# Kernel tuning notes

Hardware: AMD Instinct MI355X
Metric: run time of the kernel (lower is better)

## Reference

```python
import jax, jax.numpy as jnp
import numpy as np

NUM_LEVELS = 4
RADIUS = 4


def _avg_pool2(x):
    # x: [N, H, W] -> 2x2 avg pool, stride 2, VALID (matches F.avg_pool2d(corr, 2, 2))
    s = jax.lax.reduce_window(x, 0.0, jax.lax.add, (1, 2, 2), (1, 2, 2), 'VALID')
    return s * 0.25


def _bilinear_sampler(img, coords):
    # img: [N, H, W]; coords: [N, K, K, 2] with (x, y) in pixel units.
    # Matches grid_sample(align_corners=True, padding_mode='zeros').
    N, H, W = img.shape
    x, y = coords[..., 0], coords[..., 1]
    x0 = jnp.floor(x)
    y0 = jnp.floor(y)
    nidx = jnp.arange(N)[:, None, None]

    def corner(xi, yi, w):
        valid = (xi >= 0) & (xi <= W - 1) & (yi >= 0) & (yi <= H - 1)
        xc = jnp.clip(xi, 0, W - 1).astype(jnp.int32)
        yc = jnp.clip(yi, 0, H - 1).astype(jnp.int32)
        return jnp.where(valid, img[nidx, yc, xc], 0.0) * w

    wx1 = x - x0
    wx0 = 1.0 - wx1
    wy1 = y - y0
    wy0 = 1.0 - wy1
    return (corner(x0, y0, wx0 * wy0) + corner(x0 + 1.0, y0, wx1 * wy0)
            + corner(x0, y0 + 1.0, wx0 * wy1) + corner(x0 + 1.0, y0 + 1.0, wx1 * wy1))


def setup_inputs() -> dict:
    key = jax.random.key(0)
    ks = jax.random.split(key, 8)
    B, C, H, W, D = 2, 256, 46, 96, 256
    fmap1 = jax.random.normal(ks[0], (B, C, H, W), jnp.float32)
    fmap2 = jax.random.normal(ks[1], (B, C, H, W), jnp.float32)
    ys, xs = jnp.meshgrid(jnp.arange(H, dtype=jnp.float32),
                          jnp.arange(W, dtype=jnp.float32), indexing='ij')
    base = jnp.broadcast_to(jnp.stack([xs, ys], 0), (B, 2, H, W))  # channels = (x, y)
    coords1 = base
    coords_lookup = base + 2.0 * jax.random.normal(ks[2], (B, 2, H, W), jnp.float32)
    Wf = jax.random.normal(ks[3], (C, D), jnp.float32) / np.sqrt(C).astype(np.float32)
    bf = jnp.zeros((D,), jnp.float32)
    Wpos = jax.random.normal(ks[4], (2, D), jnp.float32) * 0.003
    Wq = jax.random.normal(ks[5], (D, D), jnp.float32) / np.sqrt(D).astype(np.float32)
    Wk = jax.random.normal(ks[6], (D, D), jnp.float32) / np.sqrt(D).astype(np.float32)
    return {"fmap1": fmap1, "fmap2": fmap2, "coords1": coords1,
            "coords_lookup": coords_lookup, "Wf": Wf, "bf": bf,
            "Wpos": Wpos, "Wq": Wq, "Wk": Wk}


def reference(fmap1, fmap2, coords1, coords_lookup, Wf, bf, Wpos, Wq, Wk):
    B, C, H, W = fmap1.shape
    HW = H * W
    D = Wf.shape[1]
    dt = fmap1.dtype
    # --- update(): SETrans cross-attention correlation volume ---
    # coords2 = gen_all_indices -> full (y, x) grid
    ys, xs = jnp.meshgrid(jnp.arange(H, dtype=dt), jnp.arange(W, dtype=dt), indexing='ij')
    coords2_yx = jnp.broadcast_to(jnp.stack([ys, xs], -1), (B, H, W, 2)).reshape(B, HW, 2)
    # coords1 stored as (x, y) channels; permute(0,2,3,1).flip(-1) -> (y, x)
    coords1_yx = jnp.transpose(coords1, (0, 2, 3, 1))[..., ::-1].reshape(B, HW, 2)
    f1 = jnp.transpose(fmap1.reshape(B, C, HW), (0, 2, 1))  # [B, HW, C]
    f2 = jnp.transpose(fmap2.reshape(B, C, HW), (0, 2, 1))
    pos1 = coords1_yx @ Wpos                                  # [B, HW, D]
    pos2 = coords2_yx @ Wpos
    vispos1 = f1 @ Wf + bf + pos1
    vispos2 = f2 @ Wf + bf + pos2
    scale = jnp.sqrt(jnp.asarray(D, dt))
    pos_biases = jnp.einsum('bid,bjd->bij', pos1, pos2) / scale  # injected positional biases
    q = vispos1 @ Wq
    k = vispos2 @ Wk
    scores = jnp.einsum('bid,bjd->bij', q, k) / scale + pos_biases
    corr = jax.nn.softmax(scores, axis=-1)                    # [B, HW1, HW2] attn-prob correlation
    corr = corr.reshape(B * HW, H, W)
    pyramid = [corr]
    for _ in range(NUM_LEVELS - 1):
        corr = _avg_pool2(corr)
        pyramid.append(corr)
    # --- __call__(coords): multiscale bilinear lookup ---
    r = RADIUS
    d = jnp.linspace(-r, r, 2 * r + 1, dtype=dt)
    dyy, dxx = jnp.meshgrid(d, d, indexing='ij')              # matches torch.meshgrid(dy, dx)
    delta = jnp.stack([dyy, dxx], -1)[None]                   # [1, K, K, 2]
    cl = jnp.transpose(coords_lookup, (0, 2, 3, 1)).reshape(B * HW, 1, 1, 2)
    outs = []
    for i, lvl in enumerate(pyramid):
        coords_lvl = cl / (2.0 ** i) + delta                  # [B*HW, K, K, 2]
        samp = _bilinear_sampler(lvl, coords_lvl)             # [B*HW, K, K]
        outs.append(samp.reshape(B, H, W, -1))
    out = jnp.concatenate(outs, axis=-1)                      # [B, H, W, L*K*K]
    return jnp.transpose(out, (0, 3, 1, 2)).astype(jnp.float32)
```

## Files before the change

kernel.cpp:

```cpp
#include <hip/hip_runtime.h>
#include <cstdint>

typedef _Float16 f16;
typedef __attribute__((ext_vector_type(2))) _Float16 f16x2;
typedef __attribute__((ext_vector_type(4))) _Float16 f16x4;
typedef __attribute__((ext_vector_type(8))) _Float16 f16x8;
typedef __attribute__((ext_vector_type(4))) float f32x4;

#define NB 2
#define NH 46
#define NW 96
#define NHW 4416
#define ND 256
#define NTILES 276
#define SSTR 4424
#define L2E 1.44269504f

#define OFF_WFQ 0
#define OFF_WFK 131072
#define OFF_PQ  262144
#define OFF_PK  264192
#define OFF_BQ  266240
#define OFF_BK  267264
#define OFF_GS  268288
#define OFF_Q   268544
#define OFF_K   4790528
#define OFF_RM  9312512
#define OFF_S   9453824
#define SCOL    4432
#define WS_NEED 87740672UL

__global__ __launch_bounds__(256) void prep_kernel(
    const float* __restrict__ Wf, const float* __restrict__ bf,
    const float* __restrict__ Wpos, const float* __restrict__ Wq,
    const float* __restrict__ Wk, char* __restrict__ ws) {
  f16* WFQ = (f16*)(ws + OFF_WFQ);
  f16* WFK = (f16*)(ws + OFF_WFK);
  float* PQ = (float*)(ws + OFF_PQ);
  float* PK = (float*)(ws + OFF_PK);
  float* BQ = (float*)(ws + OFF_BQ);
  float* BK = (float*)(ws + OFF_BK);
  float* GS = (float*)(ws + OFF_GS);
  int bid = blockIdx.x, d = threadIdx.x;
  if (bid < 256) {
    int c = bid;
    float aq = 0.f, ak = 0.f;
#pragma unroll 8
    for (int t = 0; t < 256; ++t) {
      float wf = Wf[c * 256 + t];
      aq += wf * Wq[t * 256 + d];
      ak += wf * Wk[t * 256 + d];
    }
    WFQ[c * 256 + d] = (f16)(aq * 0.0625f);
    WFK[c * 256 + d] = (f16)ak;
  } else if (bid == 256) {
    float pq0 = 0, pq1 = 0, pk0 = 0, pk1 = 0, bq = 0, bk = 0;
#pragma unroll 4
    for (int c = 0; c < 256; ++c) {
      float wq = Wq[c * 256 + d], wk = Wk[c * 256 + d];
      pq0 += Wpos[c] * wq;       pq1 += Wpos[256 + c] * wq;
      pk0 += Wpos[c] * wk;       pk1 += Wpos[256 + c] * wk;
      bq  += bf[c] * wq;         bk  += bf[c] * wk;
    }
    PQ[d] = pq0 * 0.0625f; PQ[256 + d] = pq1 * 0.0625f;
    PK[d] = pk0;           PK[256 + d] = pk1;
    BQ[d] = bq * 0.0625f;  BK[d] = bk;
  } else if (d < 4) {
    int a = d >> 1, b2 = d & 1;
    float g = 0;
    for (int t = 0; t < 256; ++t) g += Wpos[a * 256 + t] * Wpos[b2 * 256 + t];
    GS[d] = g * 0.0625f;
  }
}

__global__ __launch_bounds__(256, 2) void qk_gemm(
    const float* __restrict__ fmap1, const float* __restrict__ fmap2,
    const float* __restrict__ coords1, char* __restrict__ ws) {
  __shared__ f16 As[64 * 40];
  __shared__ f16 Bs[256 * 40];
  __shared__ float py[64], px[64];
  const int z = blockIdx.z;
  const float* fmap = z ? fmap2 : fmap1;
  const f16* Wt = (const f16*)(ws + (z ? OFF_WFK : OFF_WFQ));
  const float* P = (const float*)(ws + (z ? OFF_PK : OFF_PQ));
  const float* bias = (const float*)(ws + (z ? OFF_BK : OFF_BQ));
  f16* outb = (f16*)(ws + (z ? OFF_K : OFF_Q));
  const int t = threadIdx.x;
  const int g0 = blockIdx.x * 64;
  const int b = g0 / NHW;
  const int hwb = g0 - b * NHW;
  if (t < 64) {
    int hw = hwb + t;
    if (z == 0) {
      py[t] = coords1[(b * 2 + 1) * NHW + hw];
      px[t] = coords1[(b * 2 + 0) * NHW + hw];
    } else {
      int y = hw / NW;
      py[t] = (float)y;
      px[t] = (float)(hw - y * NW);
    }
  }
  const int lane = t & 63, wave = t >> 6;
  const int wr = (wave >> 1) * 32, wc0 = (wave & 1) * 128;
  const int hwl = t & 63, cl0 = t >> 6;
  const int dd = t & 127, ch = t >> 7;
  f32x4 acc[2][8] = {};
  for (int kt = 0; kt < 8; ++kt) {
    int kk = kt * 32;
    __syncthreads();
#pragma unroll
    for (int i = 0; i < 8; ++i) {
      int c = cl0 + i * 4;
      As[hwl * 40 + c] = (f16)fmap[(size_t)(b * ND + kk + c) * NHW + hwb + hwl];
    }
#pragma unroll
    for (int i = 0; i < 16; ++i) {
      int c = ch * 16 + i;
      Bs[dd * 40 + c] = Wt[(kk + c) * ND + dd];
      Bs[(dd + 128) * 40 + c] = Wt[(kk + c) * ND + dd + 128];
    }
    __syncthreads();
    int row = lane & 15, kq = (lane >> 4) * 8;
    f16x8 a0 = *(const f16x8*)&As[(wr + row) * 40 + kq];
    f16x8 a1 = *(const f16x8*)&As[(wr + 16 + row) * 40 + kq];
#pragma unroll
    for (int s = 0; s < 8; ++s) {
      f16x8 bs = *(const f16x8*)&Bs[(wc0 + 16 * s + row) * 40 + kq];
      acc[0][s] = __builtin_amdgcn_mfma_f32_16x16x32_f16(a0, bs, acc[0][s], 0, 0, 0);
      acc[1][s] = __builtin_amdgcn_mfma_f32_16x16x32_f16(a1, bs, acc[1][s], 0, 0, 0);
    }
  }
#pragma unroll
  for (int fi = 0; fi < 2; ++fi)
#pragma unroll
    for (int s = 0; s < 8; ++s)
#pragma unroll
      for (int r = 0; r < 4; ++r) {
        int rowl = wr + fi * 16 + (lane >> 4) * 4 + r;
        int d = wc0 + s * 16 + (lane & 15);
        float v = acc[fi][s][r] + bias[d] + py[rowl] * P[d] + px[rowl] * P[ND + d];
        outb[(size_t)(g0 + rowl) * ND + d] = (f16)v;
      }
}

__global__ __launch_bounds__(384, 1) void score_gemm(
    const float* __restrict__ coords1, char* __restrict__ ws) {
  __shared__ f16 kls[2][32][264];
  __shared__ f16 stw[6][32][36];
  __shared__ float u0s[192], u1s[192];
  const int tid = threadIdx.x;
  const int blk = blockIdx.x;
  const int xcd = blk & 7;
  const int b = xcd >> 2, nq = xcd & 3;
  const int hw0 = (blk >> 3) * 192;
  const int j00 = nq * 1104;
  const float* GS = (const float*)(ws + OFF_GS);
  if (tid < 192) {
    int hw = hw0 + tid;
    float cy = coords1[(b * 2 + 1) * NHW + hw];
    float cx = coords1[(b * 2 + 0) * NHW + hw];
    u0s[tid] = cy * GS[0] + cx * GS[2];
    u1s[tid] = cy * GS[1] + cx * GS[3];
  }
  const f16* __restrict__ qb = (const f16*)(ws + OFF_Q);
  const f16* __restrict__ kb = (const f16*)(ws + OFF_K);
  f16* __restrict__ gSb = (f16*)(ws + OFF_S) + ((size_t)b * NHW + hw0) * SCOL;
  float* __restrict__ rmG = (float*)(ws + OFF_RM);
  const int lane = tid & 63, wave = tid >> 6;
  const int q = lane & 15, h = lane >> 4;
  const int wq0 = wave * 32;
  f16x8 qfrag[2][8];
#pragma unroll
  for (int s = 0; s < 2; ++s)
#pragma unroll
    for (int ks = 0; ks < 8; ++ks)
      qfrag[s][ks] = *(const f16x8*)&qb[(size_t)(b * NHW + hw0 + wq0 + s * 16 + q) * ND + ks * 32 + h * 8];
  for (int c = tid; c < 32 * 32; c += 384) {
    int r = c >> 5, cc = c & 31;
    *(f16x8*)&kls[0][r][cc * 8] =
        *(const f16x8*)&kb[(size_t)(b * NHW + j00 + r) * ND + cc * 8];
  }
  __syncthreads();
  const float u0a = u0s[wq0 + q], u1a = u1s[wq0 + q];
  const float u0b = u0s[wq0 + 16 + q], u1b = u1s[wq0 + 16 + q];
  float pmax0 = -3e38f, pmax1 = -3e38f;
  const int srow = lane >> 1, scg = lane & 1;

  for (int it = 0; it <= 34; ++it) {
    const int buf = it & 1;
    const int jp = j00 + it * 32;
    const bool full = (it < 34);
    if (it < 34) {
      const int nW = (it < 33) ? 32 : 16;
      const int jn = j00 + (it + 1) * 32;
      for (int c = tid; c < nW * 32; c += 384) {
        int r = c >> 5, cc = c & 31;
        *(f16x8*)&kls[buf ^ 1][r][cc * 8] =
            *(const f16x8*)&kb[(size_t)(b * NHW + jn + r) * ND + cc * 8];
      }
    }
    f32x4 acc00 = {}, acc01 = {}, acc10 = {}, acc11 = {};
#pragma unroll
    for (int ks = 0; ks < 8; ++ks) {
      f16x8 kf = *(const f16x8*)&kls[buf][q][ks * 32 + h * 8];
      acc00 = __builtin_amdgcn_mfma_f32_16x16x32_f16(kf, qfrag[0][ks], acc00, 0, 0, 0);
      acc01 = __builtin_amdgcn_mfma_f32_16x16x32_f16(kf, qfrag[1][ks], acc01, 0, 0, 0);
    }
    if (full) {
#pragma unroll
      for (int ks = 0; ks < 8; ++ks) {
        f16x8 kf = *(const f16x8*)&kls[buf][16 + q][ks * 32 + h * 8];
        acc10 = __builtin_amdgcn_mfma_f32_16x16x32_f16(kf, qfrag[0][ks], acc10, 0, 0, 0);
        acc11 = __builtin_amdgcn_mfma_f32_16x16x32_f16(kf, qfrag[1][ks], acc11, 0, 0, 0);
      }
    }
    {
      float yf0[4], xf0[4];
#pragma unroll
      for (int r = 0; r < 4; ++r) {
        int j = jp + h * 4 + r;
        int yj = j / NW;
        yf0[r] = (float)yj; xf0[r] = (float)(j - yj * NW);
      }
      f16x4 va, vb;
#pragma unroll
      for (int r = 0; r < 4; ++r) {
        float s0 = acc00[r] + u0a * yf0[r] + u1a * xf0[r];
        float s1 = acc01[r] + u0b * yf0[r] + u1b * xf0[r];
        pmax0 = fmaxf(pmax0, s0);
        pmax1 = fmaxf(pmax1, s1);
        va[r] = (f16)s0; vb[r] = (f16)s1;
      }
      *(f16x4*)&stw[wave][q][h * 4] = va;
      *(f16x4*)&stw[wave][16 + q][h * 4] = vb;
      if (full) {
        float yf1[4], xf1[4];
#pragma unroll
        for (int r = 0; r < 4; ++r) {
          int j = jp + 16 + h * 4 + r;
          int yj = j / NW;
          yf1[r] = (float)yj; xf1[r] = (float)(j - yj * NW);
        }
#pragma unroll
        for (int r = 0; r < 4; ++r) {
          float s0 = acc10[r] + u0a * yf1[r] + u1a * xf1[r];
          float s1 = acc11[r] + u0b * yf1[r] + u1b * xf1[r];
          pmax0 = fmaxf(pmax0, s0);
          pmax1 = fmaxf(pmax1, s1);
          va[r] = (f16)s0; vb[r] = (f16)s1;
        }
        *(f16x4*)&stw[wave][q][16 + h * 4] = va;
        *(f16x4*)&stw[wave][16 + q][16 + h * 4] = vb;
      }
    }
    if (full) {
      f16x8 rA = *(const f16x8*)&stw[wave][srow][scg * 16];
      f16x8 rB = *(const f16x8*)&stw[wave][srow][scg * 16 + 8];
      f16* dst = &gSb[(size_t)(wq0 + srow) * SCOL + jp + scg * 16];
      *(f16x8*)&dst[0] = rA;
      *(f16x8*)&dst[8] = rB;
    } else {
      f16x8 rA = *(const f16x8*)&stw[wave][srow][scg * 8];
      *(f16x8*)&gSb[(size_t)(wq0 + srow) * SCOL + jp + scg * 8] = rA;
    }
    __syncthreads();
  }
  pmax0 = fmaxf(pmax0, __shfl_xor(pmax0, 16));
  pmax0 = fmaxf(pmax0, __shfl_xor(pmax0, 32));
  pmax1 = fmaxf(pmax1, __shfl_xor(pmax1, 16));
  pmax1 = fmaxf(pmax1, __shfl_xor(pmax1, 32));
  if (lane < 16) {
    rmG[((size_t)b * 4 + nq) * NHW + hw0 + wq0 + q] = pmax0;
    rmG[((size_t)b * 4 + nq) * NHW + hw0 + wq0 + 16 + q] = pmax1;
  }
}

__global__ __launch_bounds__(512) void lookup_kernel(
    const float* __restrict__ clup, const char* __restrict__ ws,
    float* __restrict__ out) {
  __shared__ f16 lv1W[8][1104];
  __shared__ f16 lv2W[8][264];
  __shared__ f16 lv3W[8][60];
  __shared__ f16 winW[8][10][24];
  const int tid = threadIdx.x;
  const int blk0 = blockIdx.x;
  const int xcd = blk0 & 7;
  const int b = xcd >> 2;
  const int hw0 = ((blk0 >> 3) * 4 + (xcd & 3)) * 16;
  const f16* gS = (const f16*)(ws + OFF_S);
  const float* rmG = (const float*)(ws + OFF_RM);
  const int lane = tid & 63, wave = tid >> 6;
  f16* lv1 = lv1W[wave];
  f16* lv2 = lv2W[wave];
  f16* lv3 = lv3W[wave];

  for (int rr2 = 0; rr2 < 2; ++rr2) {
    const int r = wave * 2 + rr2;
    const int hw = hw0 + r;
    const size_t grow = (size_t)b * NHW + hw;
    const f16* sp = gS + grow * SCOL;
    const float clx = clup[(b * 2 + 0) * NHW + hw];
    const float cly = clup[(b * 2 + 1) * NHW + hw];
    const float* rp = rmG + (size_t)b * 4 * NHW + hw;
    const float m = fmaxf(fmaxf(rp[0], rp[NHW]), fmaxf(rp[2 * NHW], rp[3 * NHW]));
    const int wy0 = (int)floorf(cly) - 4;
    const int wx0 = (int)floorf(clx) - 4;
    const int xb = (wx0 >> 3) << 3;
    if (lane < 30) {
      int r10 = lane / 3, chk = lane - r10 * 3;
      int yy = wy0 + r10;
      int xc = xb + chk * 8;
      if (yy >= 0 && yy < NH) {
        if (xc >= 0 && xc + 8 <= NW) {
          *(f16x8*)&winW[wave][r10][chk * 8] = *(const f16x8*)&sp[yy * NW + xc];
        } else {
#pragma unroll
          for (int e = 0; e < 8; ++e) {
            int x = xc + e;
            winW[wave][r10][chk * 8 + e] =
                (x >= 0 && x < NW) ? sp[yy * NW + x] : (f16)0.f;
          }
        }
      }
    }
    float psum = 0.f;
    for (int u = lane; u < 276; u += 64) {
      int y1 = u / 12, g = u - y1 * 12;
      f16x8 A = *(const f16x8*)&sp[(2 * y1) * NW + g * 8];
      f16x8 B = *(const f16x8*)&sp[(2 * y1 + 1) * NW + g * 8];
      f16x4 v;
#pragma unroll
      for (int e = 0; e < 4; ++e) {
        float e00 = __builtin_amdgcn_exp2f(((float)A[2 * e] - m) * L2E);
        float e01 = __builtin_amdgcn_exp2f(((float)A[2 * e + 1] - m) * L2E);
        float e10 = __builtin_amdgcn_exp2f(((float)B[2 * e] - m) * L2E);
        float e11 = __builtin_amdgcn_exp2f(((float)B[2 * e + 1] - m) * L2E);
        float s4 = (e00 + e01) + (e10 + e11);
        v[e] = (f16)s4;
        psum += s4;
      }
      *(f16x4*)&lv1[y1 * 48 + g * 4] = v;
    }
#pragma unroll
    for (int off = 1; off < 64; off <<= 1) psum += __shfl_xor(psum, off);
    const float rinv = 1.f / psum;
    __threadfence_block();
    for (int c2 = lane; c2 < 264; c2 += 64) {
      int yy = c2 / 24, xx = c2 - yy * 24;
      f16x2 a = *(const f16x2*)&lv1[(2 * yy) * 48 + 2 * xx];
      f16x2 bb = *(const f16x2*)&lv1[(2 * yy + 1) * 48 + 2 * xx];
      lv2[c2] = (f16)(((float)a[0] + (float)a[1]) + ((float)bb[0] + (float)bb[1]));
    }
    __threadfence_block();
    if (lane < 60) {
      int yy = lane / 12, xx = lane - yy * 12;
      f16x2 a = *(const f16x2*)&lv2[(2 * yy) * 24 + 2 * xx];
      f16x2 bb = *(const f16x2*)&lv2[(2 * yy + 1) * 24 + 2 * xx];
      lv3[lane] = (f16)(((float)a[0] + (float)a[1]) + ((float)bb[0] + (float)bb[1]));
    }
    __threadfence_block();
    for (int c = lane; c < 324; c += 64) {
      int lvl = c / 81, rem = c - lvl * 81;
      int k0 = rem / 9, k1 = rem - k0 * 9;
      const float wdiv[4] = {1.f, 0.25f, 0.0625f, 0.015625f};
      const int Wi[4] = {96, 48, 24, 12}, Hi[4] = {46, 23, 11, 5};
      float xq = clx / (float)(1 << lvl) + (float)(k0 - 4);
      float yq = cly / (float)(1 << lvl) + (float)(k1 - 4);
      float x0f = floorf(xq), y0f = floorf(yq);
      int x0 = (int)x0f, y0 = (int)y0f;
      float wx1 = xq - x0f, wx0f_ = 1.f - wx1;
      float wy1 = yq - y0f, wy0f_ = 1.f - wy1;
      int Wl = Wi[lvl], Hl = Hi[lvl];
      float v = 0.f;
#pragma unroll
      for (int dy = 0; dy < 2; ++dy)
#pragma unroll
        for (int dx = 0; dx < 2; ++dx) {
          int xi = x0 + dx, yi = y0 + dy;
          if (xi >= 0 && xi < Wl && yi >= 0 && yi < Hl) {
            float pv;
            if (lvl == 0)
              pv = __builtin_amdgcn_exp2f(
                  ((float)winW[wave][yi - wy0][xi - xb] - m) * L2E);
            else if (lvl == 1) pv = (float)lv1[yi * 48 + xi];
            else if (lvl == 2) pv = (float)lv2[yi * 24 + xi];
            else               pv = (float)lv3[yi * 12 + xi];
            v += pv * (dx ? wx1 : wx0f_) * (dy ? wy1 : wy0f_);
          }
        }
      int hh = hw / NW, wcol = hw - hh * NW;
      int chn = lvl * 81 + k0 * 9 + k1;
      out[((size_t)(b * 324 + chn) * NH + hh) * NW + wcol] = v * wdiv[lvl] * rinv;
    }
    __threadfence_block();
  }
}

__global__ __launch_bounds__(1024) void attn_lookup(
    const float* __restrict__ coords1, const float* __restrict__ clup,
    const char* __restrict__ ws, float* __restrict__ out) {
  __shared__ f16 S[16 * SSTR];
  __shared__ f16 lv1[4][1104];
  __shared__ f16 lv2[4][264];
  __shared__ f16 lv3[4][60];
  __shared__ float wmax[16][16];
  __shared__ float wpart[16];
  __shared__ float u0s[16], u1s[16], clxs[16], clys[16], rinv[16], rowmaxS[16];
  const int tid = threadIdx.x;
  const int blk0 = blockIdx.x;
  const int xcd = blk0 & 7;
  const int b = xcd >> 2;
  const int hw0 = ((blk0 >> 3) * 4 + (xcd & 3)) * 16;
  const float* GS = (const float*)(ws + OFF_GS);
  if (tid < 16) {
    int hw = hw0 + tid;
    float cy = coords1[(b * 2 + 1) * NHW + hw];
    float cx = coords1[(b * 2 + 0) * NHW + hw];
    u0s[tid] = cy * GS[0] + cx * GS[2];
    u1s[tid] = cy * GS[1] + cx * GS[3];
    clxs[tid] = clup[(b * 2 + 0) * NHW + hw];
    clys[tid] = clup[(b * 2 + 1) * NHW + hw];
  }
  const f16* qb = (const f16*)(ws + OFF_Q);
  const f16* kb = (const f16*)(ws + OFF_K);
  const int lane = tid & 63;
  const int arow = lane & 15, akq = (lane >> 4) * 8;
  const int i0 = (lane >> 4) * 4;
  f16x8 afrag[8];
#pragma unroll
  for (int ks = 0; ks < 8; ++ks)
    afrag[ks] = *(const f16x8*)&qb[(size_t)(b * NHW + hw0 + arow) * ND + ks * 32 + akq];
  __syncthreads();
  float u0r[4], u1r[4];
#pragma unroll
  for (int r = 0; r < 4; ++r) { u0r[r] = u0s[i0 + r]; u1r[r] = u1s[i0 + r]; }
  const int wave = tid >> 6;
  float pmax[4] = {-3e38f, -3e38f, -3e38f, -3e38f};
  {
    const int cnt = (NTILES - wave + 15) / 16;
    const f16* kp = &kb[(size_t)(b * NHW + wave * 16 + arow) * ND + akq];
    const size_t tstep = (size_t)256 * ND;
    int nt = wave;
    f16x8 h0[4], h1[4];
#pragma unroll
    for (int s = 0; s < 4; ++s) h0[s] = *(const f16x8*)&kp[s * 32];
    for (int i = 0; i < cnt; ++i) {
      f32x4 acc0 = {}, acc1 = {};
#pragma unroll
      for (int s = 0; s < 4; ++s) h1[s] = *(const f16x8*)&kp[128 + s * 32];
      acc0 = __builtin_amdgcn_mfma_f32_16x16x32_f16(afrag[0], h0[0], acc0, 0, 0, 0);
      acc1 = __builtin_amdgcn_mfma_f32_16x16x32_f16(afrag[1], h0[1], acc1, 0, 0, 0);
      acc0 = __builtin_amdgcn_mfma_f32_16x16x32_f16(afrag[2], h0[2], acc0, 0, 0, 0);
      acc1 = __builtin_amdgcn_mfma_f32_16x16x32_f16(afrag[3], h0[3], acc1, 0, 0, 0);
      const f16* kpn = kp + tstep;
      if (i + 1 < cnt) {
#pragma unroll
        for (int s = 0; s < 4; ++s) h0[s] = *(const f16x8*)&kpn[s * 32];
      }
      acc0 = __builtin_amdgcn_mfma_f32_16x16x32_f16(afrag[4], h1[0], acc0, 0, 0, 0);
      acc1 = __builtin_amdgcn_mfma_f32_16x16x32_f16(afrag[5], h1[1], acc1, 0, 0, 0);
      acc0 = __builtin_amdgcn_mfma_f32_16x16x32_f16(afrag[6], h1[2], acc0, 0, 0, 0);
      acc1 = __builtin_amdgcn_mfma_f32_16x16x32_f16(afrag[7], h1[3], acc1, 0, 0, 0);
      int j = nt * 16 + (lane & 15);
      int yj = j / NW;
      float yf = (float)yj, xf = (float)(j - yj * NW);
#pragma unroll
      for (int r = 0; r < 4; ++r) {
        float s = acc0[r] + acc1[r] + u0r[r] * yf + u1r[r] * xf;
        pmax[r] = fmaxf(pmax[r], s);
        S[(i0 + r) * SSTR + j] = (f16)s;
      }
      kp = kpn; nt += 16;
    }
  }
#pragma unroll
  for (int off = 1; off < 16; off <<= 1)
#pragma unroll
    for (int r = 0; r < 4; ++r) pmax[r] = fmaxf(pmax[r], __shfl_xor(pmax[r], off));
  if ((lane & 15) == 0) {
#pragma unroll
    for (int r = 0; r < 4; ++r) wmax[wave][i0 + r] = pmax[r];
  }
  __syncthreads();
  if (tid < 16) {
    float m = wmax[0][tid];
#pragma unroll
    for (int w = 1; w < 16; ++w) m = fmaxf(m, wmax[w][tid]);
    rowmaxS[tid] = m;
  }
  __syncthreads();
  const int rgrp = tid >> 8, ts = tid & 255;
  for (int p = 0; p < 4; ++p) {
    const int r = p * 4 + rgrp;
    const f16* Sr = &S[r * SSTR];
    const float m = rowmaxS[r];
    float psum = 0.f;
    for (int c = ts; c < 1104; c += 256) {
      int yy = c / 48, xx = c - yy * 48;
      f16x2 a = *(const f16x2*)&Sr[(2 * yy) * NW + 2 * xx];
      f16x2 bb = *(const f16x2*)&Sr[(2 * yy + 1) * NW + 2 * xx];
      float e0 = __builtin_amdgcn_exp2f(((float)a[0] - m) * L2E);
      float e1 = __builtin_amdgcn_exp2f(((float)a[1] - m) * L2E);
      float e2 = __builtin_amdgcn_exp2f(((float)bb[0] - m) * L2E);
      float e3 = __builtin_amdgcn_exp2f(((float)bb[1] - m) * L2E);
      float s4 = (e0 + e1) + (e2 + e3);
      lv1[rgrp][c] = (f16)s4;
      psum += s4;
    }
#pragma unroll
    for (int off = 1; off < 64; off <<= 1) psum += __shfl_xor(psum, off);
    if (lane == 0) wpart[tid >> 6] = psum;
    __syncthreads();
    if (tid < 4)
      rinv[p * 4 + tid] = 1.f / (((wpart[tid * 4] + wpart[tid * 4 + 1]) +
                                  (wpart[tid * 4 + 2] + wpart[tid * 4 + 3])));
    for (int c2 = ts; c2 < 264; c2 += 256) {
      int yy = c2 / 24, xx = c2 - yy * 24;
      f16x2 a = *(const f16x2*)&lv1[rgrp][(2 * yy) * 48 + 2 * xx];
      f16x2 bb = *(const f16x2*)&lv1[rgrp][(2 * yy + 1) * 48 + 2 * xx];
      lv2[rgrp][c2] = (f16)(((float)a[0] + (float)a[1]) + ((float)bb[0] + (float)bb[1]));
    }
    __syncthreads();
    if (ts < 60) {
      int yy = ts / 12, xx = ts - yy * 12;
      f16x2 a = *(const f16x2*)&lv2[rgrp][(2 * yy) * 24 + 2 * xx];
      f16x2 bb = *(const f16x2*)&lv2[rgrp][(2 * yy + 1) * 24 + 2 * xx];
      lv3[rgrp][ts] = (f16)(((float)a[0] + (float)a[1]) + ((float)bb[0] + (float)bb[1]));
    }
    __syncthreads();
    for (int idx = tid; idx < 1296; idx += 1024) {
      int rl = idx / 324, c = idx - rl * 324;
      int rr = p * 4 + rl;
      int lvl = c / 81, rem = c - lvl * 81;
      int k0 = rem / 9, k1 = rem - k0 * 9;
      const float wdiv[4] = {1.f, 0.25f, 0.0625f, 0.015625f};
      const int Wi[4] = {96, 48, 24, 12}, Hi[4] = {46, 23, 11, 5};
      float m2 = rowmaxS[rr];
      float xq = clxs[rr] / (float)(1 << lvl) + (float)(k0 - 4);
      float yq = clys[rr] / (float)(1 << lvl) + (float)(k1 - 4);
      float x0f = floorf(xq), y0f = floorf(yq);
      int x0 = (int)x0f, y0 = (int)y0f;
      float wx1 = xq - x0f, wx0 = 1.f - wx1;
      float wy1 = yq - y0f, wy0 = 1.f - wy1;
      int Wl = Wi[lvl], Hl = Hi[lvl];
      float v = 0.f;
#pragma unroll
      for (int dy = 0; dy < 2; ++dy)
#pragma unroll
        for (int dx = 0; dx < 2; ++dx) {
          int xi = x0 + dx, yi = y0 + dy;
          if (xi >= 0 && xi < Wl && yi >= 0 && yi < Hl) {
            float pv;
            if (lvl == 0)
              pv = __builtin_amdgcn_exp2f(((float)S[rr * SSTR + yi * NW + xi] - m2) * L2E);
            else if (lvl == 1) pv = (float)lv1[rl][yi * 48 + xi];
            else if (lvl == 2) pv = (float)lv2[rl][yi * 24 + xi];
            else               pv = (float)lv3[rl][yi * 12 + xi];
            v += pv * (dx ? wx1 : wx0) * (dy ? wy1 : wy0);
          }
        }
      int hw = hw0 + rr;
      int h = hw / NW, w = hw - h * NW;
      int chn = lvl * 81 + k0 * 9 + k1;
      out[((size_t)(b * 324 + chn) * NH + h) * NW + w] = v * wdiv[lvl] * rinv[rr];
    }
    __syncthreads();
  }
}

extern "C" void kernel_launch(void* const* d_in, const int* in_sizes, int n_in,
                              void* d_out, int out_size, void* d_ws, size_t ws_size,
                              hipStream_t stream) {
  const float* fmap1 = (const float*)d_in[0];
  const float* fmap2 = (const float*)d_in[1];
  const float* coords1 = (const float*)d_in[2];
  const float* clup = (const float*)d_in[3];
  const float* Wf = (const float*)d_in[4];
  const float* bf = (const float*)d_in[5];
  const float* Wpos = (const float*)d_in[6];
  const float* Wq = (const float*)d_in[7];
  const float* Wk = (const float*)d_in[8];
  char* ws = (char*)d_ws;
  float* out = (float*)d_out;

  prep_kernel<<<dim3(258), dim3(256), 0, stream>>>(Wf, bf, Wpos, Wq, Wk, ws);
  qk_gemm<<<dim3(138, 1, 2), dim3(256), 0, stream>>>(fmap1, fmap2, coords1, ws);
  if (ws_size >= (size_t)WS_NEED) {
    score_gemm<<<dim3(23 * 8), dim3(384), 0, stream>>>(coords1, ws);
    lookup_kernel<<<dim3(NB * NTILES), dim3(512), 0, stream>>>(clup, ws, out);
  } else {
    attn_lookup<<<dim3(NB * NTILES), dim3(1024), 0, stream>>>(coords1, clup, ws, out);
  }
}
```

Baseline: 145.6 us.

## Split score GEMM key range into eight segments and store row maxima inline

The score GEMM grid doubles from 184 to 368 blocks by splitting each batch's key columns into eight uneven tile ranges instead of four. Launch bounds now allow two blocks per CU, which should fill more of the device. The per-segment row maxima are written into padding columns of the score row rather than a separate buffer, so the lookup kernel reads them next to the scores it already loads. In exchange, each block repeats the Q-fragment loads and prologue, and the code assumes SCOL has spare space past column 4416.

```diff
diff --git a/kernel.cpp b/kernel.cpp
--- a/kernel.cpp
+++ b/kernel.cpp
@@ -143,17 +143,20 @@
       }
 }
 
-__global__ __launch_bounds__(384, 1) void score_gemm(
+__global__ __launch_bounds__(384, 2) void score_gemm(
     const float* __restrict__ coords1, char* __restrict__ ws) {
   __shared__ f16 kls[2][32][264];
   __shared__ f16 stw[6][32][36];
   __shared__ float u0s[192], u1s[192];
   const int tid = threadIdx.x;
   const int blk = blockIdx.x;
-  const int xcd = blk & 7;
-  const int b = xcd >> 2, nq = xcd & 3;
-  const int hw0 = (blk >> 3) * 192;
-  const int j00 = nq * 1104;
+  const int comb = blk & 15;
+  const int b = comb >> 3, ns = comb & 7;
+  const int hw0 = (blk >> 4) * 192;
+  const int sstart[9] = {0, 17, 34, 51, 68, 85, 102, 120, 138};
+  const int t0s = sstart[ns];
+  const int cnt = sstart[ns + 1] - t0s;
+  const int j00 = t0s * 32;
   const float* GS = (const float*)(ws + OFF_GS);
   if (tid < 192) {
     int hw = hw0 + tid;
@@ -165,7 +168,6 @@
   const f16* __restrict__ qb = (const f16*)(ws + OFF_Q);
   const f16* __restrict__ kb = (const f16*)(ws + OFF_K);
   f16* __restrict__ gSb = (f16*)(ws + OFF_S) + ((size_t)b * NHW + hw0) * SCOL;
-  float* __restrict__ rmG = (float*)(ws + OFF_RM);
   const int lane = tid & 63, wave = tid >> 6;
   const int q = lane & 15, h = lane >> 4;
   const int wq0 = wave * 32;
@@ -186,14 +188,12 @@
   float pmax0 = -3e38f, pmax1 = -3e38f;
   const int srow = lane >> 1, scg = lane & 1;
 
-  for (int it = 0; it <= 34; ++it) {
+  for (int it = 0; it < cnt; ++it) {
     const int buf = it & 1;
     const int jp = j00 + it * 32;
-    const bool full = (it < 34);
-    if (it < 34) {
-      const int nW = (it < 33) ? 32 : 16;
+    if (it + 1 < cnt) {
       const int jn = j00 + (it + 1) * 32;
-      for (int c = tid; c < nW * 32; c += 384) {
+      for (int c = tid; c < 1024; c += 384) {
         int r = c >> 5, cc = c & 31;
         *(f16x8*)&kls[buf ^ 1][r][cc * 8] =
             *(const f16x8*)&kb[(size_t)(b * NHW + jn + r) * ND + cc * 8];
@@ -206,21 +206,22 @@
       acc00 = __builtin_amdgcn_mfma_f32_16x16x32_f16(kf, qfrag[0][ks], acc00, 0, 0, 0);
       acc01 = __builtin_amdgcn_mfma_f32_16x16x32_f16(kf, qfrag[1][ks], acc01, 0, 0, 0);
     }
-    if (full) {
-#pragma unroll
-      for (int ks = 0; ks < 8; ++ks) {
-        f16x8 kf = *(const f16x8*)&kls[buf][16 + q][ks * 32 + h * 8];
-        acc10 = __builtin_amdgcn_mfma_f32_16x16x32_f16(kf, qfrag[0][ks], acc10, 0, 0, 0);
-        acc11 = __builtin_amdgcn_mfma_f32_16x16x32_f16(kf, qfrag[1][ks], acc11, 0, 0, 0);
-      }
+#pragma unroll
+    for (int ks = 0; ks < 8; ++ks) {
+      f16x8 kf = *(const f16x8*)&kls[buf][16 + q][ks * 32 + h * 8];
+      acc10 = __builtin_amdgcn_mfma_f32_16x16x32_f16(kf, qfrag[0][ks], acc10, 0, 0, 0);
+      acc11 = __builtin_amdgcn_mfma_f32_16x16x32_f16(kf, qfrag[1][ks], acc11, 0, 0, 0);
     }
     {
-      float yf0[4], xf0[4];
+      float yf0[4], xf0[4], yf1[4], xf1[4];
 #pragma unroll
       for (int r = 0; r < 4; ++r) {
         int j = jp + h * 4 + r;
         int yj = j / NW;
         yf0[r] = (float)yj; xf0[r] = (float)(j - yj * NW);
+        int j1 = jp + 16 + h * 4 + r;
+        int yj1 = j1 / NW;
+        yf1[r] = (float)yj1; xf1[r] = (float)(j1 - yj1 * NW);
       }
       f16x4 va, vb;
 #pragma unroll
@@ -233,35 +234,23 @@
       }
       *(f16x4*)&stw[wave][q][h * 4] = va;
       *(f16x4*)&stw[wave][16 + q][h * 4] = vb;
-      if (full) {
-        float yf1[4], xf1[4];
-#pragma unroll
-        for (int r = 0; r < 4; ++r) {
-          int j = jp + 16 + h * 4 + r;
-          int yj = j / NW;
-          yf1[r] = (float)yj; xf1[r] = (float)(j - yj * NW);
-        }
-#pragma unroll
-        for (int r = 0; r < 4; ++r) {
-          float s0 = acc10[r] + u0a * yf1[r] + u1a * xf1[r];
-          float s1 = acc11[r] + u0b * yf1[r] + u1b * xf1[r];
-          pmax0 = fmaxf(pmax0, s0);
-          pmax1 = fmaxf(pmax1, s1);
-          va[r] = (f16)s0; vb[r] = (f16)s1;
-        }
-        *(f16x4*)&stw[wave][q][16 + h * 4] = va;
-        *(f16x4*)&stw[wave][16 + q][16 + h * 4] = vb;
-      }
-    }
-    if (full) {
+#pragma unroll
+      for (int r = 0; r < 4; ++r) {
+        float s0 = acc10[r] + u0a * yf1[r] + u1a * xf1[r];
+        float s1 = acc11[r] + u0b * yf1[r] + u1b * xf1[r];
+        pmax0 = fmaxf(pmax0, s0);
+        pmax1 = fmaxf(pmax1, s1);
+        va[r] = (f16)s0; vb[r] = (f16)s1;
+      }
+      *(f16x4*)&stw[wave][q][16 + h * 4] = va;
+      *(f16x4*)&stw[wave][16 + q][16 + h * 4] = vb;
+    }
+    {
       f16x8 rA = *(const f16x8*)&stw[wave][srow][scg * 16];
       f16x8 rB = *(const f16x8*)&stw[wave][srow][scg * 16 + 8];
       f16* dst = &gSb[(size_t)(wq0 + srow) * SCOL + jp + scg * 16];
       *(f16x8*)&dst[0] = rA;
       *(f16x8*)&dst[8] = rB;
-    } else {
-      f16x8 rA = *(const f16x8*)&stw[wave][srow][scg * 8];
-      *(f16x8*)&gSb[(size_t)(wq0 + srow) * SCOL + jp + scg * 8] = rA;
     }
     __syncthreads();
   }
@@ -270,8 +259,8 @@
   pmax1 = fmaxf(pmax1, __shfl_xor(pmax1, 16));
   pmax1 = fmaxf(pmax1, __shfl_xor(pmax1, 32));
   if (lane < 16) {
-    rmG[((size_t)b * 4 + nq) * NHW + hw0 + wq0 + q] = pmax0;
-    rmG[((size_t)b * 4 + nq) * NHW + hw0 + wq0 + 16 + q] = pmax1;
+    *(float*)&gSb[(size_t)(wq0 + q) * SCOL + 4416 + ns * 2] = pmax0;
+    *(float*)&gSb[(size_t)(wq0 + 16 + q) * SCOL + 4416 + ns * 2] = pmax1;
   }
 }
 
@@ -288,7 +277,6 @@
   const int b = xcd >> 2;
   const int hw0 = ((blk0 >> 3) * 4 + (xcd & 3)) * 16;
   const f16* gS = (const f16*)(ws + OFF_S);
-  const float* rmG = (const float*)(ws + OFF_RM);
   const int lane = tid & 63, wave = tid >> 6;
   f16* lv1 = lv1W[wave];
   f16* lv2 = lv2W[wave];
@@ -301,8 +289,10 @@
     const f16* sp = gS + grow * SCOL;
     const float clx = clup[(b * 2 + 0) * NHW + hw];
     const float cly = clup[(b * 2 + 1) * NHW + hw];
-    const float* rp = rmG + (size_t)b * 4 * NHW + hw;
-    const float m = fmaxf(fmaxf(rp[0], rp[NHW]), fmaxf(rp[2 * NHW], rp[3 * NHW]));
+    const float* rp = (const float*)&sp[4416];
+    float m = rp[0];
+#pragma unroll
+    for (int k = 1; k < 8; ++k) m = fmaxf(m, rp[k]);
     const int wy0 = (int)floorf(cly) - 4;
     const int wx0 = (int)floorf(clx) - 4;
     const int xb = (wx0 >> 3) << 3;
@@ -586,7 +576,7 @@
   prep_kernel<<<dim3(258), dim3(256), 0, stream>>>(Wf, bf, Wpos, Wq, Wk, ws);
   qk_gemm<<<dim3(138, 1, 2), dim3(256), 0, stream>>>(fmap1, fmap2, coords1, ws);
   if (ws_size >= (size_t)WS_NEED) {
-    score_gemm<<<dim3(23 * 8), dim3(384), 0, stream>>>(coords1, ws);
+    score_gemm<<<dim3(23 * 16), dim3(384), 0, stream>>>(coords1, ws);
     lookup_kernel<<<dim3(NB * NTILES), dim3(512), 0, stream>>>(clup, ws, out);
   } else {
     attn_lookup<<<dim3(NB * NTILES), dim3(1024), 0, stream>>>(coords1, clup, ws, out);
```

Result: slower. 158.4 us (+8.8%).
